# Optimization experiments

Measured on AMD Instinct MI355X. Metric: run time of the kernel, lower is better.

Reference implementation:

```python
import jax, jax.numpy as jnp
import numpy as np

INF = 1e30  # sentinel for 'unreached' cost
MAX_ITERS = 512


def setup_inputs() -> dict:
    key = jax.random.key(0)
    img = jax.random.uniform(key, (3, 2048, 2048), dtype=jnp.float32)
    return {"img": img}


def _sobel_mag(gray):
    # gray: [H,W] -> gradient magnitude [H,W] (the 'processing_filter')
    kx = jnp.array([[-1.0, 0.0, 1.0], [-2.0, 0.0, 2.0], [-1.0, 0.0, 1.0]], gray.dtype)
    k = jnp.stack([kx, kx.T])[:, None]  # [2,1,3,3]
    g = jax.lax.conv_general_dilated(gray[None, None], k, (1, 1), 'SAME')[0]  # [2,H,W]
    return jnp.sqrt(g[0] ** 2 + g[1] ** 2)


def _neighbor_min(c):
    # min over 4-connected neighbors, INF padding at borders
    big_r = jnp.full((1, c.shape[1]), INF, c.dtype)
    big_c = jnp.full((c.shape[0], 1), INF, c.dtype)
    n = jnp.concatenate([big_r, c[:-1]], 0)
    s = jnp.concatenate([c[1:], big_r], 0)
    w = jnp.concatenate([big_c, c[:, :-1]], 1)
    e = jnp.concatenate([c[:, 1:], big_c], 1)
    return jnp.minimum(jnp.minimum(n, s), jnp.minimum(w, e))


def _relax(cost, img):
    # minimax-path (flood-level) relaxation: cost[p] = min(cost[p], max(min_nbr_cost, img[p]))
    return jnp.minimum(cost, jnp.maximum(_neighbor_min(cost), img))


def _watershed2(img, markers):
    # marker-based watershed on topography `img` with labels {1,2}.
    # Label of p = argmin over seed sets of the minimax path cost (flooding level),
    # which matches skimage.segmentation.watershed region assignment (4-connectivity).
    c1 = jnp.where(markers == 1, img, jnp.float32(INF))
    c2 = jnp.where(markers == 2, img, jnp.float32(INF))

    def cond(st):
        _, _, i, ch = st
        return jnp.logical_and(ch, i < MAX_ITERS)

    def body(st):
        c1, c2, i, _ = st
        n1 = _relax(c1, img)
        n2 = _relax(c2, img)
        ch = jnp.logical_or(jnp.any(n1 < c1), jnp.any(n2 < c2))
        return n1, n2, i + 1, ch

    c1, c2, _, _ = jax.lax.while_loop(cond, body, (c1, c2, jnp.int32(0), jnp.bool_(True)))
    return jnp.where(c2 < c1, jnp.float32(2.0), jnp.float32(1.0))


def _forward(img):
    gray = jnp.einsum('chw,c->hw', img, jnp.array([0.2989, 0.587, 0.114], img.dtype))
    filter_res = _sobel_mag(gray)  # [H,W]
    q_hi = jnp.quantile(filter_res, 0.9925)
    q_lo = jnp.quantile(filter_res, 0.9825)
    # torch sets 2 first, then 1, so pixels satisfying both end up as 1
    markers = jnp.where(filter_res <= q_lo, 1, jnp.where(filter_res >= q_hi, 2, 0))
    labels = _watershed2(gray, markers)[None]  # [1,H,W], values in {1,2}
    labels = labels - labels.min()
    return labels / labels.max()


def reference(img):
    return _forward(img)
```

## Files before the change

### kernel.cpp

```cpp
#include <hip/hip_runtime.h>
#include <hip/hip_cooperative_groups.h>

#define HH 2048
#define WW 2048
#define NPX (HH*WW)
#define INFV 1e30f
#define TS 128
#define NT 16
#define NTL 256
#define CY 32

namespace cg = cooperative_groups;

__device__ __forceinline__ void BARL(){
  __builtin_amdgcn_sched_barrier(0);
  asm volatile("s_waitcnt lgkmcnt(0)" ::: "memory");
  __builtin_amdgcn_s_barrier();
  __builtin_amdgcn_sched_barrier(0);
}

__device__ __forceinline__ float sobel_at(const float* __restrict__ g, int y, int x){
  float a00,a01,a02,a10,a12,a20,a21,a22;
  if (y>0 && y<HH-1 && x>0 && x<WW-1){
    const float* p = g + (size_t)(y-1)*WW + x;
    a00=p[-1]; a01=p[0]; a02=p[1];
    p += WW;   a10=p[-1];          a12=p[1];
    p += WW;   a20=p[-1]; a21=p[0]; a22=p[1];
  } else {
    auto at=[&](int yy,int xx)->float{
      return (yy<0||yy>=HH||xx<0||xx>=WW)?0.0f:g[(size_t)yy*WW+xx];
    };
    a00=at(y-1,x-1); a01=at(y-1,x); a02=at(y-1,x+1);
    a10=at(y,  x-1);                a12=at(y,  x+1);
    a20=at(y+1,x-1); a21=at(y+1,x); a22=at(y+1,x+1);
  }
  float gx = __fadd_rn(__fadd_rn(__fsub_rn(a02,a00), __fmul_rn(2.0f,__fsub_rn(a12,a10))), __fsub_rn(a22,a20));
  float gy = __fadd_rn(__fadd_rn(__fsub_rn(a20,a00), __fmul_rn(2.0f,__fsub_rn(a21,a01))), __fsub_rn(a22,a02));
  return sqrtf(__fadd_rn(__fmul_rn(gx,gx),__fmul_rn(gy,gy)));
}

__global__ void gray_kernel(const float* __restrict__ img, float* __restrict__ gray){
  const float* R=img; const float* G=img+NPX; const float* B=img+2*(size_t)NPX;
  for (int i=blockIdx.x*blockDim.x+threadIdx.x; i<NPX; i+=gridDim.x*blockDim.x){
    gray[i] = __fadd_rn(__fadd_rn(__fmul_rn(0.2989f,R[i]),__fmul_rn(0.587f,G[i])),__fmul_rn(0.114f,B[i]));
  }
}

__global__ void sobel_hist1(const float* __restrict__ gray, float* __restrict__ fr,
                            unsigned* __restrict__ hist){
  __shared__ unsigned h[4*2048];
  for (int i=threadIdx.x;i<4*2048;i+=blockDim.x) h[i]=0;
  __syncthreads();
  const int rep=(threadIdx.x&3)*2048;
  for (int i=blockIdx.x*blockDim.x+threadIdx.x; i<NPX; i+=gridDim.x*blockDim.x){
    int y=i>>11, x=i&(WW-1);
    float f=sobel_at(gray,y,x);
    fr[i]=f;
    unsigned key=__float_as_uint(f);
    atomicAdd(&h[rep+(key>>21)],1u);
  }
  __syncthreads();
  for (int i=threadIdx.x;i<2048;i+=blockDim.x){
    unsigned s=h[i]+h[i+2048]+h[i+4096]+h[i+6144];
    if (s) atomicAdd(&hist[i],s);
  }
}

__global__ void hist_l2(const float* __restrict__ fr, const unsigned* __restrict__ sel1,
                        unsigned* __restrict__ hist2){
  __shared__ unsigned h[4*2048];
  __shared__ unsigned sb[4];
  if (threadIdx.x<4) sb[threadIdx.x]=sel1[threadIdx.x];
  for (int i=threadIdx.x;i<4*2048;i+=blockDim.x) h[i]=0;
  __syncthreads();
  for (int i=blockIdx.x*blockDim.x+threadIdx.x; i<NPX; i+=gridDim.x*blockDim.x){
    unsigned key=__float_as_uint(fr[i]);
    unsigned b=key>>21, sub=(key>>10)&0x7FFu;
    #pragma unroll
    for (int k=0;k<4;++k) if (b==sb[k]) atomicAdd(&h[k*2048+sub],1u);
  }
  __syncthreads();
  for (int i=threadIdx.x;i<4*2048;i+=blockDim.x){ unsigned s=h[i]; if (s) atomicAdd(&hist2[i],s); }
}

__global__ void hist_l3(const float* __restrict__ fr, const unsigned* __restrict__ sel1,
                        const unsigned* __restrict__ sel2, unsigned* __restrict__ hist3){
  __shared__ unsigned h[4*1024];
  __shared__ unsigned pf[4];
  if (threadIdx.x<4) pf[threadIdx.x]=(sel1[threadIdx.x]<<11)|sel2[threadIdx.x];
  for (int i=threadIdx.x;i<4*1024;i+=blockDim.x) h[i]=0;
  __syncthreads();
  for (int i=blockIdx.x*blockDim.x+threadIdx.x; i<NPX; i+=gridDim.x*blockDim.x){
    unsigned key=__float_as_uint(fr[i]);
    unsigned p22=key>>10, sub=key&0x3FFu;
    #pragma unroll
    for (int k=0;k<4;++k) if (p22==pf[k]) atomicAdd(&h[k*1024+sub],1u);
  }
  __syncthreads();
  for (int i=threadIdx.x;i<4*1024;i+=blockDim.x){ unsigned s=h[i]; if (s) atomicAdd(&hist3[i],s); }
}

__global__ void scan_l1(const unsigned* __restrict__ hist, unsigned* __restrict__ sel1,
                        unsigned* __restrict__ rem1){
  __shared__ unsigned part[1024];
  const int t=threadIdx.x;
  unsigned a=hist[2*t], b=hist[2*t+1];
  part[t]=a+b; __syncthreads();
  for (int off=1;off<1024;off<<=1){
    unsigned add=(t>=off)?part[t-off]:0u; __syncthreads();
    part[t]+=add; __syncthreads();
  }
  unsigned before=(t>0)?part[t-1]:0u;
  const unsigned R[4]={4120902u,4120903u,4162845u,4162846u};
  unsigned cum=before;
  #pragma unroll
  for (int i=0;i<4;++i) if (R[i]>=cum && R[i]<cum+a){ sel1[i]=2*t;   rem1[i]=R[i]-cum; }
  cum+=a;
  #pragma unroll
  for (int i=0;i<4;++i) if (R[i]>=cum && R[i]<cum+b){ sel1[i]=2*t+1; rem1[i]=R[i]-cum; }
}

__global__ void scan_l2(const unsigned* __restrict__ hist2, const unsigned* __restrict__ rem1,
                        unsigned* __restrict__ sel2, unsigned* __restrict__ rem2){
  __shared__ unsigned part[1024];
  const int t=threadIdx.x;
  for (int i=0;i<4;++i){
    const unsigned* hh=hist2+i*2048;
    unsigned a=hh[2*t], b=hh[2*t+1];
    part[t]=a+b; __syncthreads();
    for (int off=1;off<1024;off<<=1){
      unsigned add=(t>=off)?part[t-off]:0u; __syncthreads();
      part[t]+=add; __syncthreads();
    }
    unsigned before=(t>0)?part[t-1]:0u;
    unsigned r=rem1[i], cum=before;
    if (r>=cum && r<cum+a){ sel2[i]=2*t;   rem2[i]=r-cum; }
    cum+=a;
    if (r>=cum && r<cum+b){ sel2[i]=2*t+1; rem2[i]=r-cum; }
    __syncthreads();
  }
}

__global__ void scan_l3(const unsigned* __restrict__ hist3, const unsigned* __restrict__ sel1,
                        const unsigned* __restrict__ sel2, const unsigned* __restrict__ rem2,
                        float* __restrict__ scal){
  __shared__ unsigned part[1024];
  __shared__ float vals[4];
  const int t=threadIdx.x;
  for (int i=0;i<4;++i){
    unsigned c=hist3[i*1024+t];
    part[t]=c; __syncthreads();
    for (int off=1;off<1024;off<<=1){
      unsigned add=(t>=off)?part[t-off]:0u; __syncthreads();
      part[t]+=add; __syncthreads();
    }
    unsigned before=(t>0)?part[t-1]:0u;
    unsigned r=rem2[i];
    if (r>=before && r<before+c){
      unsigned key=(sel1[i]<<21)|(sel2[i]<<10)|(unsigned)t;
      vals[i]=__uint_as_float(key);
    }
    __syncthreads();
  }
  if (t==0){
    scal[0]=__fadd_rn(__fmul_rn(vals[0],0.25f),__fmul_rn(vals[1],0.75f));
    scal[1]=__fadd_rn(__fmul_rn(vals[2],0.25f),__fmul_rn(vals[3],0.75f));
  }
}

__global__ void init_cost(const float* __restrict__ gray, const float* frbuf,
                          const float* __restrict__ scal,
                          float* c1out, float* __restrict__ c2out){
  const float qlo=scal[0], qhi=scal[1];
  for (int i=blockIdx.x*blockDim.x+threadIdx.x; i<NPX; i+=gridDim.x*blockDim.x){
    float f=frbuf[i];
    float g=gray[i];
    bool m1 = (f<=qlo);
    bool m2 = (!m1) && (f>=qhi);
    c1out[i] = m1 ? g : INFV;
    c2out[i] = (m1|m2) ? g : INFV;
  }
}


#define HSCAN_LR(va,vb,gA,gB,hl) do{ \
  float ql_=gA[j], qh_=va[j]; \
  qh_=fminf(vb[j],fmaxf(gB[j],qh_)); ql_=fmaxf(gB[j],ql_); \
  _Pragma("unroll") \
  for (int d_=1;d_<64;d_<<=1){ \
    float pl_=__shfl_up(ql_,(unsigned)d_), ph_=__shfl_up(qh_,(unsigned)d_); \
    if (c>=d_){ qh_=fminf(qh_,fmaxf(ql_,ph_)); ql_=fmaxf(ql_,pl_); } \
  } \
  float E_=fminf(qh_,fmaxf(ql_,(hl))); \
  float In_=__shfl_up(E_,1u); if(c==0) In_=(hl); \
  float na_=fminf(va[j],fmaxf(gA[j],In_)); if(na_<va[j]){va[j]=na_;ch=true;} \
  float nb_=fminf(vb[j],fmaxf(gB[j],na_)); if(nb_<vb[j]){vb[j]=nb_;ch=true;} \
}while(0)

#define HSCAN_RL(va,vb,gA,gB,hr) do{ \
  float ql_=gB[j], qh_=vb[j]; \
  qh_=fminf(va[j],fmaxf(gA[j],qh_)); ql_=fmaxf(gA[j],ql_); \
  _Pragma("unroll") \
  for (int d_=1;d_<64;d_<<=1){ \
    float pl_=__shfl_down(ql_,(unsigned)d_), ph_=__shfl_down(qh_,(unsigned)d_); \
    if (c+d_<64){ qh_=fminf(qh_,fmaxf(ql_,ph_)); ql_=fmaxf(ql_,pl_); } \
  } \
  float E_=fminf(qh_,fmaxf(ql_,(hr))); \
  float In_=__shfl_down(E_,1u); if(c==63) In_=(hr); \
  float nb_=fminf(vb[j],fmaxf(gB[j],In_)); if(nb_<vb[j]){vb[j]=nb_;ch=true;} \
  float na_=fminf(va[j],fmaxf(gA[j],nb_)); if(na_<va[j]){va[j]=na_;ch=true;} \
}while(0)

#define VCOMP_DN(va,gA,Larr,Harr,XX) { float ql_=gA[0], qh_=va[0]; \
  _Pragma("unroll") for (int jj_=1;jj_<8;++jj_){ qh_=fminf(va[jj_],fmaxf(gA[jj_],qh_)); ql_=fmaxf(gA[jj_],ql_);} \
  Larr[w][XX]=ql_; Harr[w][XX]=qh_; }

#define VCOMP_UP(va,gA,Larr,Harr,XX) { float ql_=gA[7], qh_=va[7]; \
  _Pragma("unroll") for (int jj_=6;jj_>=0;--jj_){ qh_=fminf(va[jj_],fmaxf(gA[jj_],qh_)); ql_=fmaxf(gA[jj_],ql_);} \
  Larr[w][XX]=ql_; Harr[w][XX]=qh_; }

#define VAPPLY_DN(va,gA,Larr,XX) { float In_=Larr[w][XX]; \
  _Pragma("unroll") for (int jj_=0;jj_<8;++jj_){ float nv_=fminf(va[jj_],fmaxf(In_,gA[jj_])); if(nv_<va[jj_]){va[jj_]=nv_;ch=true;} In_=nv_; } }

#define VAPPLY_UP(va,gA,Larr,XX) { float In_=Larr[w][XX]; \
  _Pragma("unroll") for (int jj_=7;jj_>=0;--jj_){ float nv_=fminf(va[jj_],fmaxf(In_,gA[jj_])); if(nv_<va[jj_]){va[jj_]=nv_;ch=true;} In_=nv_; } }

#define CHAIN_DN(Harr,Larr,HT) { float E=HALO[HT][x]; \
  _Pragma("unroll") for (int b_=0;b_<16;++b_){ float I=E; E=fminf(Harr[b_][x],fmaxf(Larr[b_][x],I)); Larr[b_][x]=I; } }

#define CHAIN_UP(Harr,Larr,HB) { float E=HALO[HB][x]; \
  _Pragma("unroll") for (int b_=15;b_>=0;--b_){ float I=E; E=fminf(Harr[b_][x],fmaxf(Larr[b_][x],I)); Larr[b_][x]=I; } }

#define CHAINC_DN(Harr,Larr,Earr,HT,ECHV) { \
  float E=HALO[HT][x]; unsigned m_=0; \
  _Pragma("unroll") for (int b_=0;b_<16;++b_){ \
    float I_=E; E=fminf(Harr[b_][x],fmaxf(Larr[b_][x],I_)); \
    if (__any(I_!=Earr[b_][x])) m_|=(1u<<b_); \
    Earr[b_][x]=I_; } \
  if (c==0 && m_) atomicOr(&ECHV,(int)m_); }

#define CHAINC_UP(Harr,Larr,Earr,HB,ECHV) { \
  float E=HALO[HB][x]; unsigned m_=0; \
  _Pragma("unroll") for (int b_=15;b_>=0;--b_){ \
    float I_=E; E=fminf(Harr[b_][x],fmaxf(Larr[b_][x],I_)); \
    if (__any(I_!=Earr[b_][x])) m_|=(1u<<b_); \
    Earr[b_][x]=I_; } \
  if (c==0 && m_) atomicOr(&ECHV,(int)m_); }

#define HFIELD(va,vb,IHL,IHR) do{ \
  _Pragma("unroll") \
  for (int j=0;j<8;++j){ \
    const int r_=(w<<3)|j; \
    const float hl=HALO[IHL][r_], hr=HALO[IHR][r_]; \
    { float la_=__shfl_up(vb[j],1u); if(c==0) la_=hl; \
      bool p_=__any((fminf(va[j],fmaxf(la_,ga[j]))<va[j])||(fminf(vb[j],fmaxf(va[j],gb[j]))<vb[j])); \
      if (p_){ HSCAN_LR(va,vb,ga,gb,hl); } } \
    { float ra_=__shfl_down(va[j],1u); if(c==63) ra_=hr; \
      bool p_=__any((fminf(vb[j],fmaxf(ra_,gb[j]))<vb[j])||(fminf(va[j],fmaxf(vb[j],ga[j]))<va[j])); \
      if (p_){ HSCAN_RL(va,vb,ga,gb,hr); } } \
  } \
}while(0)

#define ASTORE(p,v) __hip_atomic_store((p),(v),__ATOMIC_RELAXED,__HIP_MEMORY_SCOPE_AGENT)
#define ALOAD(p)    __hip_atomic_load((p),__ATOMIC_RELAXED,__HIP_MEMORY_SCOPE_AGENT)

__global__ void __launch_bounds__(1024,4)
tile_solve(float* __restrict__ c1g, float* __restrict__ cg, const float* __restrict__ grayg)
{
  __shared__ float DNL1[16][128], DNH1[16][128], DNL2[16][128], DNH2[16][128];
  __shared__ float UPL1[16][128], UPH1[16][128], UPL2[16][128], UPH2[16][128];
  __shared__ float HALO[8][128];
  __shared__ int VN1[2],HN1[2],VN2[2],HN2[2];
  const int tid=threadIdx.x, w=tid>>6, c=tid&63;
  const int oty=blockIdx.x>>5, otx=blockIdx.x&31;
  const int wy0=oty*64-32, wx0=otx*64-32, x0=c<<1;
  HALO[tid>>7][tid&127]=INFV;
  if (tid==0){ VN1[0]=1;HN1[0]=1;VN2[0]=1;HN2[0]=1;
               VN1[1]=0;HN1[1]=0;VN2[1]=0;HN2[1]=0; }
  float v1a[8],v1b[8],v2a[8],v2b[8],ga[8],gb[8];
  const int gx=wx0+x0;
  const bool cok=(gx>=0)&&(gx+1<WW);
  #pragma unroll
  for (int j=0;j<8;++j){
    const int gy=wy0+(w<<3)+j;
    const bool rok=(gy>=0)&&(gy<HH);
    if (rok&&cok){
      const size_t b=(size_t)gy*WW+gx;
      float2 t1=*(const float2*)(c1g+b);
      float2 t2=*(const float2*)(cg+b);
      float2 tg=*(const float2*)(grayg+b);
      v1a[j]=t1.x; v1b[j]=t1.y; v2a[j]=t2.x; v2b[j]=t2.y; ga[j]=tg.x; gb[j]=tg.y;
    } else if (rok){
      const bool aok=(gx>=0)&&(gx<WW), bok=(gx+1>=0)&&(gx+1<WW);
      const size_t b=(size_t)gy*WW;
      v1a[j]=aok?c1g[b+gx]:INFV;   v1b[j]=bok?c1g[b+gx+1]:INFV;
      v2a[j]=aok?cg [b+gx]:INFV;   v2b[j]=bok?cg [b+gx+1]:INFV;
      ga [j]=aok?grayg[b+gx]:INFV; gb [j]=bok?grayg[b+gx+1]:INFV;
    } else {
      v1a[j]=INFV;v1b[j]=INFV;v2a[j]=INFV;v2b[j]=INFV;ga[j]=INFV;gb[j]=INFV;
    }
  }
  __syncthreads();
  for (int cyc=0; cyc<64; ++cyc){
    const int cur=cyc&1, nxt=cur^1;
    const int vn1=VN1[cur], hn1=HN1[cur], vn2=VN2[cur], hn2=HN2[cur];
    if (!(vn1|hn1|vn2|hn2)) break;
    if (vn1){
      VCOMP_DN(v1a,ga,DNL1,DNH1,x0) VCOMP_DN(v1b,gb,DNL1,DNH1,x0+1)
      VCOMP_UP(v1a,ga,UPL1,UPH1,x0) VCOMP_UP(v1b,gb,UPL1,UPH1,x0+1)
    }
    if (vn2){
      VCOMP_DN(v2a,ga,DNL2,DNH2,x0) VCOMP_DN(v2b,gb,DNL2,DNH2,x0+1)
      VCOMP_UP(v2a,ga,UPL2,UPH2,x0) VCOMP_UP(v2b,gb,UPL2,UPH2,x0+1)
    }
    __syncthreads();
    if (w<8){
      const int x=((w&1)<<6)|c;
      const bool go=(w>>2)?(vn2!=0):(vn1!=0);
      if (go){
        switch(w>>1){
          case 0: CHAIN_DN(DNH1,DNL1,0) break;
          case 1: CHAIN_UP(UPH1,UPL1,2) break;
          case 2: CHAIN_DN(DNH2,DNL2,1) break;
          default:CHAIN_UP(UPH2,UPL2,3) break;
        }
      }
    }
    __syncthreads();
    if (vn1){ bool ch=false;
      VAPPLY_DN(v1a,ga,DNL1,x0) VAPPLY_DN(v1b,gb,DNL1,x0+1)
      VAPPLY_UP(v1a,ga,UPL1,x0) VAPPLY_UP(v1b,gb,UPL1,x0+1)
      if (ch) HN1[nxt]=1;
    }
    if (hn1){ bool ch=false;
      HFIELD(v1a,v1b,4,6);
      if (ch) VN1[nxt]=1;
    }
    if (vn2){ bool ch=false;
      VAPPLY_DN(v2a,ga,DNL2,x0) VAPPLY_DN(v2b,gb,DNL2,x0+1)
      VAPPLY_UP(v2a,ga,UPL2,x0) VAPPLY_UP(v2b,gb,UPL2,x0+1)
      if (ch) HN2[nxt]=1;
    }
    if (hn2){ bool ch=false;
      HFIELD(v2a,v2b,5,7);
      if (ch) VN2[nxt]=1;
    }
    if (tid==0){ VN1[cur]=0; HN1[cur]=0; VN2[cur]=0; HN2[cur]=0; }
    __syncthreads();
  }
  if (w>=4 && w<12 && c>=16 && c<48){
    #pragma unroll
    for (int j=0;j<8;++j){
      const int gy=wy0+(w<<3)+j;
      const size_t b=(size_t)gy*WW+gx;
      float2 o1; o1.x=v1a[j]; o1.y=v1b[j];
      float2 o2; o2.x=v2a[j]; o2.y=v2b[j];
      *(float2*)(c1g+b)=o1;
      *(float2*)(cg +b)=o2;
    }
  }
}

#define CYCLE(HV,CUR,NXT) do{ \
  if (hsrc){ \
    if (HV < HALO[harr][hx]){ \
      HALO[harr][hx]=HV; \
      if (harr<4){ if (harr&1) VN2[NXT]=1; else VN1[NXT]=1; } \
      else       { if (harr&1) HN2[NXT]=1; else HN1[NXT]=1; } \
    } \
    HV=ALOAD(hsrc); \
  } \
  const int vn1=VN1[CUR], hn1=HN1[CUR], vn2=VN2[CUR], hn2=HN2[CUR]; \
  const unsigned vd1=(unsigned)VD1s, vd2=(unsigned)VD2s; \
  if (!(vn1|hn1|vn2|hn2|(int)(vd1|vd2))){ \
    BARL(); \
  } else { \
     \
    if ((vd1>>w)&1){ \
      VCOMP_DN(v1a,ga,DNL1,DNH1,x0) VCOMP_DN(v1b,gb,DNL1,DNH1,x0+1) \
      VCOMP_UP(v1a,ga,UPL1,UPH1,x0) VCOMP_UP(v1b,gb,UPL1,UPH1,x0+1) \
    } \
    if ((vd2>>w)&1){ \
      VCOMP_DN(v2a,ga,DNL2,DNH2,x0) VCOMP_DN(v2b,gb,DNL2,DNH2,x0+1) \
      VCOMP_UP(v2a,ga,UPL2,UPH2,x0) VCOMP_UP(v2b,gb,UPL2,UPH2,x0+1) \
    } \
    if (tid==0){ ECH1s=0; ECH2s=0; } \
    BARL(); \
     \
    if (w<8){ \
      const int x=((w&1)<<6)|c; \
      switch(w>>1){ \
        case 0: if (vn1|(int)vd1) CHAINC_DN(DNH1,DNL1,EDN1,0,ECH1s) break; \
        case 1: if (vn1|(int)vd1) CHAINC_UP(UPH1,UPL1,EUP1,2,ECH1s) break; \
        case 2: if (vn2|(int)vd2) CHAINC_DN(DNH2,DNL2,EDN2,1,ECH2s) break; \
        default:if (vn2|(int)vd2) CHAINC_UP(UPH2,UPL2,EUP2,3,ECH2s) break; \
      } \
    } \
    if (tid==0){ VD1s=0; VD2s=0; } \
    BARL(); \
     \
    const unsigned am1=((unsigned)ECH1s)|vd1, am2=((unsigned)ECH2s)|vd2; \
    bool pf1=false, pf2=false; \
    { bool ch=false; \
      if ((am1>>w)&1){ \
        VAPPLY_DN(v1a,ga,EDN1,x0) VAPPLY_DN(v1b,gb,EDN1,x0+1) \
        VAPPLY_UP(v1a,ga,EUP1,x0) VAPPLY_UP(v1b,gb,EUP1,x0+1) \
      } \
      bool vch=__any(ch); \
      ch=false; \
      if (hn1){ HFIELD(v1a,v1b,4,6); } \
      bool hch=__any(ch); \
      if ((vch|hch) && c==0) atomicOr(&VD1s,1<<w); \
      if (vch) HN1[NXT]=1; \
      pf1 = vch|hch; \
    } \
    { bool ch=false; \
      if ((am2>>w)&1){ \
        VAPPLY_DN(v2a,ga,EDN2,x0) VAPPLY_DN(v2b,gb,EDN2,x0+1) \
        VAPPLY_UP(v2a,ga,EUP2,x0) VAPPLY_UP(v2b,gb,EUP2,x0+1) \
      } \
      bool vch=__any(ch); \
      ch=false; \
      if (hn2){ HFIELD(v2a,v2b,5,7); } \
      bool hch=__any(ch); \
      if ((vch|hch) && c==0) atomicOr(&VD2s,1<<w); \
      if (vch) HN2[NXT]=1; \
      pf2 = vch|hch; \
    } \
    if (pf1|pf2){ \
      if (w==0){ const int eb=(tile*4+0)*128; \
        if(pf1){ ASTORE(EB1+eb+x0,v1a[0]); ASTORE(EB1+eb+x0+1,v1b[0]); } \
        if(pf2){ ASTORE(EB2+eb+x0,v2a[0]); ASTORE(EB2+eb+x0+1,v2b[0]); } } \
      if (w==15){ const int eb=(tile*4+1)*128; \
        if(pf1){ ASTORE(EB1+eb+x0,v1a[7]); ASTORE(EB1+eb+x0+1,v1b[7]); } \
        if(pf2){ ASTORE(EB2+eb+x0,v2a[7]); ASTORE(EB2+eb+x0+1,v2b[7]); } } \
      if (c==0){ const int eb=(tile*4+2)*128+(w<<3); \
        _Pragma("unroll") \
        for (int j=0;j<8;++j){ if(pf1)ASTORE(EB1+eb+j,v1a[j]); if(pf2)ASTORE(EB2+eb+j,v2a[j]); } } \
      if (c==63){ const int eb=(tile*4+3)*128+(w<<3); \
        _Pragma("unroll") \
        for (int j=0;j<8;++j){ if(pf1)ASTORE(EB1+eb+j,v1b[j]); if(pf2)ASTORE(EB2+eb+j,v2b[j]); } } \
      if (c==1) wflag=1; \
    } \
    if (tid==0){ VN1[CUR]=0; HN1[CUR]=0; VN2[CUR]=0; HN2[CUR]=0; } \
    BARL(); \
  } \
}while(0)

__global__ void __launch_bounds__(1024,4)
ws_solve(float* __restrict__ c1g, const float* __restrict__ grayg, float* outg,
         int* __restrict__ flagIt)
{
  __shared__ float DNL1[16][128], DNH1[16][128], DNL2[16][128], DNH2[16][128];
  __shared__ float UPL1[16][128], UPH1[16][128], UPL2[16][128], UPH2[16][128];
  __shared__ float EDN1[16][128], EUP1[16][128], EDN2[16][128], EUP2[16][128];
  __shared__ float HALO[8][128];
  __shared__ int VN1[2],HN1[2],VN2[2],HN2[2];
  __shared__ int VD1s, VD2s, ECH1s, ECH2s;
  __shared__ int wflag;
  cg::grid_group grid = cg::this_grid();
  const int tid=threadIdx.x, w=tid>>6, c=tid&63;
  const int xcd=blockIdx.x&7, idx=blockIdx.x>>3;
  const int tx=((xcd&3)<<2)|(idx&3), ty=((xcd>>2)<<3)|(idx>>2);
  const int tile=ty*NT+tx;
  const int by=ty*TS, bx=tx*TS, x0=c<<1;
  float* EB1=outg;
  float* EB2=outg+(NTL*4*128);

  const int hx=tid&127, harr=tid>>7;
  const float* hsrc=nullptr;
  {
    const float* EB=(harr&1)?EB2:EB1;
    switch(harr>>1){
      case 0: if (ty>0)    hsrc=EB+((tile-NT)*4+1)*128+hx; break;
      case 1: if (ty<NT-1) hsrc=EB+((tile+NT)*4+0)*128+hx; break;
      case 2: if (tx>0)    hsrc=EB+((tile-1)*4+3)*128+hx;  break;
      default:if (tx<NT-1) hsrc=EB+((tile+1)*4+2)*128+hx;  break;
    }
  }

  float v1a[8],v1b[8],v2a[8],v2b[8],ga[8],gb[8];
  {
    size_t base=(size_t)(by+(w<<3))*WW + bx + x0;
    #pragma unroll
    for (int j=0;j<8;++j){
      float2 t1=*(const float2*)(c1g+base);
      float2 t2=*(const float2*)(outg+base);
      float2 tg=*(const float2*)(grayg+base);
      v1a[j]=t1.x; v1b[j]=t1.y; v2a[j]=t2.x; v2b[j]=t2.y; ga[j]=tg.x; gb[j]=tg.y;
      base+=(size_t)WW;
    }
  }
  grid.sync();

  if (w==0){ const int eb=(tile*4+0)*128;
    ASTORE(EB1+eb+x0,v1a[0]); ASTORE(EB1+eb+x0+1,v1b[0]);
    ASTORE(EB2+eb+x0,v2a[0]); ASTORE(EB2+eb+x0+1,v2b[0]); }
  if (w==15){ const int eb=(tile*4+1)*128;
    ASTORE(EB1+eb+x0,v1a[7]); ASTORE(EB1+eb+x0+1,v1b[7]);
    ASTORE(EB2+eb+x0,v2a[7]); ASTORE(EB2+eb+x0+1,v2b[7]); }
  if (c==0){ const int eb=(tile*4+2)*128+(w<<3);
    #pragma unroll
    for (int j=0;j<8;++j){ ASTORE(EB1+eb+j,v1a[j]); ASTORE(EB2+eb+j,v2a[j]); } }
  if (c==63){ const int eb=(tile*4+3)*128+(w<<3);
    #pragma unroll
    for (int j=0;j<8;++j){ ASTORE(EB1+eb+j,v1b[j]); ASTORE(EB2+eb+j,v2b[j]); } }
  HALO[harr][hx]=INFV;
  if (tid==0){ VN1[0]=1;HN1[0]=1;VN2[0]=1;HN2[0]=1;
               VN1[1]=0;HN1[1]=0;VN2[1]=0;HN2[1]=0;
               VD1s=0xFFFF; VD2s=0xFFFF; ECH1s=0; ECH2s=0; wflag=0; }
  __threadfence();
  grid.sync();

  float hvA=INFV, hvB=INFV;
  if (hsrc){ hvA=ALOAD(hsrc); hvB=ALOAD(hsrc); }

  for (int win=0; win<96; ++win){
    for (int cyc=0; cyc<CY; cyc+=2){
      CYCLE(hvA,0,1);
      CYCLE(hvB,1,0);
    }
    if (tid==0 && (wflag || (VD1s|VD2s))) atomicMax(flagIt,win+1);
    __threadfence();
    grid.sync();
    int fv=ALOAD(flagIt);
    if (fv<=win) break;
    if (tid==0) wflag=0;
    __syncthreads();
  }
  {
    size_t base=(size_t)(by+(w<<3))*WW + bx + x0;
    #pragma unroll
    for (int j=0;j<8;++j){
      float2 o; o.x=(v2a[j]<v1a[j])?1.0f:0.0f; o.y=(v2b[j]<v1b[j])?1.0f:0.0f;
      *(float2*)(outg+base)=o;
      base+=(size_t)WW;
    }
  }
}

extern "C" void kernel_launch(void* const* d_in, const int* in_sizes, int n_in,
                              void* d_out, int out_size, void* d_ws, size_t ws_size,
                              hipStream_t stream)
{
  const float* img=(const float*)d_in[0];
  float* out=(float*)d_out;
  char* wsb=(char*)d_ws;
  float* gray=(float*)wsb;
  float* c1  =(float*)(wsb + (size_t)NPX*4);
  unsigned* meta=(unsigned*)(wsb + (size_t)NPX*8);
  float* c2 = out;

  unsigned* hist1=meta;
  unsigned* hist2=meta+2048;
  unsigned* hist3=meta+10240;
  unsigned* sel1 =meta+14336;
  unsigned* rem1 =meta+14340;
  unsigned* sel2 =meta+14344;
  unsigned* rem2 =meta+14348;
  float*    scal =(float*)(meta+14352);
  int*      flagIt=(int*)(meta+14354);

  hipMemsetAsync(meta, 0, 14355*sizeof(unsigned), stream);
  hipLaunchKernelGGL(gray_kernel, dim3(4096), dim3(256), 0, stream, img, gray);
  hipLaunchKernelGGL(sobel_hist1, dim3(1024), dim3(256), 0, stream, gray, c1, hist1);
  hipLaunchKernelGGL(scan_l1, dim3(1), dim3(1024), 0, stream, hist1, sel1, rem1);
  hipLaunchKernelGGL(hist_l2, dim3(1024), dim3(256), 0, stream, c1, sel1, hist2);
  hipLaunchKernelGGL(scan_l2, dim3(1), dim3(1024), 0, stream, hist2, rem1, sel2, rem2);
  hipLaunchKernelGGL(hist_l3, dim3(1024), dim3(256), 0, stream, c1, sel1, sel2, hist3);
  hipLaunchKernelGGL(scan_l3, dim3(1), dim3(1024), 0, stream, hist3, sel1, sel2, rem2, scal);
  hipLaunchKernelGGL(init_cost, dim3(4096), dim3(256), 0, stream, gray, c1, scal, c1, c2);

  hipLaunchKernelGGL(tile_solve, dim3(1024), dim3(1024), 0, stream, c1, c2, gray);

  void* args[]={ (void*)&c1,(void*)&gray,(void*)&out,(void*)&flagIt };
  (void)hipLaunchCooperativeKernel(ws_solve, dim3(NTL), dim3(1024), args, 0, stream);
}
```

Before: 578.4 us.

## Fuse marker initialization and Sobel recompute into tile_solve, cap tile cycles

Removes the init_cost kernel and has tile_solve compute the Sobel magnitude and marker thresholds inline from gray, building the initial cost values in registers. This drops a full-image pass that read the filter buffer and wrote c1/c2, at the cost of redundant stencil loads in the overlapping tile windows. It also lowers the tile-local relaxation cycle cap from 64 to 24, leaving more convergence work to the global cooperative solver. It relies on tile_solve writing c1/c2 back for ws_solve, since they are no longer produced beforehand.

```diff
diff --git a/kernel.cpp b/kernel.cpp
--- a/kernel.cpp
+++ b/kernel.cpp
@@ -168,20 +168,6 @@
   }
 }
 
-__global__ void init_cost(const float* __restrict__ gray, const float* frbuf,
-                          const float* __restrict__ scal,
-                          float* c1out, float* __restrict__ c2out){
-  const float qlo=scal[0], qhi=scal[1];
-  for (int i=blockIdx.x*blockDim.x+threadIdx.x; i<NPX; i+=gridDim.x*blockDim.x){
-    float f=frbuf[i];
-    float g=gray[i];
-    bool m1 = (f<=qlo);
-    bool m2 = (!m1) && (f>=qhi);
-    c1out[i] = m1 ? g : INFV;
-    c2out[i] = (m1|m2) ? g : INFV;
-  }
-}
-
 
 #define HSCAN_LR(va,vb,gA,gB,hl) do{ \
   float ql_=gA[j], qh_=va[j]; \
@@ -265,7 +251,8 @@
 #define ALOAD(p)    __hip_atomic_load((p),__ATOMIC_RELAXED,__HIP_MEMORY_SCOPE_AGENT)
 
 __global__ void __launch_bounds__(1024,4)
-tile_solve(float* __restrict__ c1g, float* __restrict__ cg, const float* __restrict__ grayg)
+tile_solve(float* __restrict__ c1g, float* __restrict__ cg,
+           const float* __restrict__ grayg, const float* __restrict__ scal)
 {
   __shared__ float DNL1[16][128], DNH1[16][128], DNL2[16][128], DNH2[16][128];
   __shared__ float UPL1[16][128], UPH1[16][128], UPL2[16][128], UPH2[16][128];
@@ -274,34 +261,30 @@
   const int tid=threadIdx.x, w=tid>>6, c=tid&63;
   const int oty=blockIdx.x>>5, otx=blockIdx.x&31;
   const int wy0=oty*64-32, wx0=otx*64-32, x0=c<<1;
+  const float qlo=scal[0], qhi=scal[1];
   HALO[tid>>7][tid&127]=INFV;
   if (tid==0){ VN1[0]=1;HN1[0]=1;VN2[0]=1;HN2[0]=1;
                VN1[1]=0;HN1[1]=0;VN2[1]=0;HN2[1]=0; }
   float v1a[8],v1b[8],v2a[8],v2b[8],ga[8],gb[8];
   const int gx=wx0+x0;
-  const bool cok=(gx>=0)&&(gx+1<WW);
   #pragma unroll
   for (int j=0;j<8;++j){
     const int gy=wy0+(w<<3)+j;
     const bool rok=(gy>=0)&&(gy<HH);
-    if (rok&&cok){
-      const size_t b=(size_t)gy*WW+gx;
-      float2 t1=*(const float2*)(c1g+b);
-      float2 t2=*(const float2*)(cg+b);
-      float2 tg=*(const float2*)(grayg+b);
-      v1a[j]=t1.x; v1b[j]=t1.y; v2a[j]=t2.x; v2b[j]=t2.y; ga[j]=tg.x; gb[j]=tg.y;
-    } else if (rok){
-      const bool aok=(gx>=0)&&(gx<WW), bok=(gx+1>=0)&&(gx+1<WW);
-      const size_t b=(size_t)gy*WW;
-      v1a[j]=aok?c1g[b+gx]:INFV;   v1b[j]=bok?c1g[b+gx+1]:INFV;
-      v2a[j]=aok?cg [b+gx]:INFV;   v2b[j]=bok?cg [b+gx+1]:INFV;
-      ga [j]=aok?grayg[b+gx]:INFV; gb [j]=bok?grayg[b+gx+1]:INFV;
-    } else {
-      v1a[j]=INFV;v1b[j]=INFV;v2a[j]=INFV;v2b[j]=INFV;ga[j]=INFV;gb[j]=INFV;
-    }
-  }
-  __syncthreads();
-  for (int cyc=0; cyc<64; ++cyc){
+    const bool aok=rok&&(gx>=0)&&(gx<WW), bok=rok&&(gx+1>=0)&&(gx+1<WW);
+    float gA=INFV,gB=INFV,fA=0.0f,fB=0.0f;
+    if (aok){ gA=grayg[(size_t)gy*WW+gx];   fA=sobel_at(grayg,gy,gx); }
+    if (bok){ gB=grayg[(size_t)gy*WW+gx+1]; fB=sobel_at(grayg,gy,gx+1); }
+    ga[j]=gA; gb[j]=gB;
+    if (aok){ bool m1=(fA<=qlo); bool m2=(!m1)&&(fA>=qhi);
+              v1a[j]=m1?gA:INFV; v2a[j]=(m1|m2)?gA:INFV; }
+    else    { v1a[j]=INFV; v2a[j]=INFV; }
+    if (bok){ bool m1=(fB<=qlo); bool m2=(!m1)&&(fB>=qhi);
+              v1b[j]=m1?gB:INFV; v2b[j]=(m1|m2)?gB:INFV; }
+    else    { v1b[j]=INFV; v2b[j]=INFV; }
+  }
+  __syncthreads();
+  for (int cyc=0; cyc<24; ++cyc){
     const int cur=cyc&1, nxt=cur^1;
     const int vn1=VN1[cur], hn1=HN1[cur], vn2=VN2[cur], hn2=HN2[cur];
     if (!(vn1|hn1|vn2|hn2)) break;
@@ -569,9 +552,8 @@
   hipLaunchKernelGGL(scan_l2, dim3(1), dim3(1024), 0, stream, hist2, rem1, sel2, rem2);
   hipLaunchKernelGGL(hist_l3, dim3(1024), dim3(256), 0, stream, c1, sel1, sel2, hist3);
   hipLaunchKernelGGL(scan_l3, dim3(1), dim3(1024), 0, stream, hist3, sel1, sel2, rem2, scal);
-  hipLaunchKernelGGL(init_cost, dim3(4096), dim3(256), 0, stream, gray, c1, scal, c1, c2);
-
-  hipLaunchKernelGGL(tile_solve, dim3(1024), dim3(1024), 0, stream, c1, c2, gray);
+
+  hipLaunchKernelGGL(tile_solve, dim3(1024), dim3(1024), 0, stream, c1, c2, gray, scal);
 
   void* args[]={ (void*)&c1,(void*)&gray,(void*)&out,(void*)&flagIt };
   (void)hipLaunchCooperativeKernel(ws_solve, dim3(NTL), dim3(1024), args, 0, stream);
```

New measurement: 597.0 us. +3.2%, slower.
